# Kernel optimization log

Measured on AMD Instinct MI355X. Metric: run time of the kernel, lower is better.

Reference implementation:

```python
import jax, jax.numpy as jnp
import numpy as np

N = 100000   # nodes per graph
E = 1600000  # edges (avg degree 16)
B = 2        # num_graph (batch)
F_IN = 116   # num_input
EMB = 12     # embedding dim
H = 128      # hidden_size


def setup_inputs() -> dict:
    key = jax.random.key(0)
    ks = jax.random.split(key, 8)
    node = jax.random.normal(ks[0], (B, N, F_IN), dtype=jnp.float32)
    node_type = jax.random.randint(ks[1], (N,), 0, 8, dtype=jnp.int32)
    edge_index = jax.random.randint(ks[2], (2, E), 0, N, dtype=jnp.int32)
    embed = jax.random.normal(ks[3], (8, EMB), dtype=jnp.float32)
    d1 = F_IN + EMB
    W1 = jax.random.normal(ks[4], (d1, H), dtype=jnp.float32) / np.sqrt(d1)
    b1 = jnp.zeros((H,), dtype=jnp.float32)
    W2 = jax.random.normal(ks[5], (H, H), dtype=jnp.float32) / np.sqrt(H)
    b2 = jnp.zeros((H,), dtype=jnp.float32)
    return {"node": node, "node_type": node_type, "edge_index": edge_index,
            "embed": embed, "W1": W1, "b1": b1, "W2": W2, "b2": b2}


def _gcn_conv(x, src, dst, W, b):
    """PyG GCNConv: symmetric norm with self-loops, linear (no lin bias), bias after agg.
    x: [B, N, F]; src/dst: [E] int; W: [F, H]; b: [H]."""
    n = x.shape[1]
    # degree over (A + I), computed on destination nodes
    deg = jnp.zeros((n,), x.dtype).at[dst].add(1.0) + 1.0
    dis = jax.lax.rsqrt(deg)  # deg^{-1/2}
    xw = jnp.einsum('bnf,fh->bnh', x, W)          # [B, N, H]
    norm = dis[src] * dis[dst]                    # [E]
    msgs = xw[:, src, :] * norm[None, :, None]    # [B, E, H]
    agg = jax.vmap(lambda m: jax.ops.segment_sum(m, dst, num_segments=n))(msgs)
    agg = agg + xw * (dis * dis)[None, :, None]   # self-loop contribution
    return agg + b


def reference(node, node_type, edge_index, embed, W1, b1, W2, b2):
    src, dst = edge_index[0], edge_index[1]
    emb = embed[node_type]                                      # [N, EMB]
    b = node.shape[0]
    emb_b = jnp.broadcast_to(emb[None], (b,) + emb.shape)       # repeat over batch
    x = jnp.concatenate([node, emb_b], axis=2)                  # [B, N, F_IN+EMB]
    x = jax.nn.relu(_gcn_conv(x, src, dst, W1, b1))
    # F.dropout in eval mode is identity
    x = _gcn_conv(x, src, dst, W2, b2)
    return jnp.mean(x, axis=1)                                  # [B, H]
```

## Files before the change

kernel.cpp:

```cpp
#include <hip/hip_runtime.h>
#include <stdint.h>

typedef unsigned int uint32;
typedef unsigned short ushort16;
typedef __attribute__((ext_vector_type(8))) short bf16x8;
typedef __attribute__((ext_vector_type(4))) float f32x4;
typedef __attribute__((ext_vector_type(2))) float f32x2;

#define F_IN 116
#define HID  128
#define EMBD 12
#define IDX24 0x00FFFFFFu
#define BCAP 4608
#define PCAP 8448

__device__ __forceinline__ uint32 f2bf(float f) {
    uint32 x = __float_as_uint(f);
    return (x + 0x7fffu + ((x >> 16) & 1u)) >> 16;
}

__global__ void k_setup(const float* __restrict__ W1, ushort16* __restrict__ W1s,
                        int* __restrict__ bcurD, int* __restrict__ bcurS,
                        float* __restrict__ partial, uint32* __restrict__ xwzrow,
                        int* __restrict__ csrz, int N, int K) {
    int tid = blockIdx.x * 256 + threadIdx.x;
    if (tid < K) { bcurD[tid] = tid * BCAP; bcurS[tid] = tid * BCAP; }
    if (blockIdx.x == 0) {
        partial[threadIdx.x] = 0.f;
        if (threadIdx.x < 64) xwzrow[threadIdx.x] = 0u;
        if (threadIdx.x < 16) csrz[threadIdx.x] = N;
    }
    if (tid < 2048) {
        int q = tid & 3, n = (tid >> 2) & 15, t = (tid >> 6) & 7, kc = (tid >> 9) & 3;
        int chunk = ((kc * 8 + t) * 64 + n * 4 + q);
        int h = ((n >> 2) << 5) + t * 4 + (n & 3);
#pragma unroll
        for (int j = 0; j < 8; ++j) {
            int k = kc * 32 + q * 8 + j;
            W1s[chunk * 8 + j] = (ushort16)f2bf(W1[k * HID + h]);
        }
    }
}

__global__ __launch_bounds__(256) void k_bin(
    const int* __restrict__ src, const int* __restrict__ dst,
    int* __restrict__ bcurD, int* __restrict__ bcurS,
    uint32* __restrict__ ebufD, uint32* __restrict__ ebufS, int E) {
    __shared__ int lhD[512], lbD[512], lhS[512], lbS[512];
    const int tid = threadIdx.x;
    const int e0 = blockIdx.x * 4096;
    const int eend = min(e0 + 4096, E);
    for (int i = tid; i < 512; i += 256) { lhD[i] = 0; lhS[i] = 0; }
    __syncthreads();
    for (int e = e0 + tid; e < eend; e += 256) {
        atomicAdd(&lhD[dst[e] >> 8], 1);
        atomicAdd(&lhS[src[e] >> 8], 1);
    }
    __syncthreads();
    const int rot = (blockIdx.x * 277) & 511;
#pragma unroll
    for (int i = 0; i < 2; ++i) {
        int k = (rot + tid + i * 256) & 511;
        int c = lhD[k]; lbD[k] = c ? atomicAdd(&bcurD[k], c) : 0; lhD[k] = 0;
        int d = lhS[k]; lbS[k] = d ? atomicAdd(&bcurS[k], d) : 0; lhS[k] = 0;
    }
    __syncthreads();
    for (int e = e0 + tid; e < eend; e += 256) {
        int s = src[e], d = dst[e];
        int bkD = d >> 8;
        int p = lbD[bkD] + atomicAdd(&lhD[bkD], 1);
        if (p < (bkD + 1) * BCAP) ebufD[p] = ((uint32)(d & 255) << 24) | (uint32)s;
        int bkS = s >> 8;
        int p2 = lbS[bkS] + atomicAdd(&lhS[bkS], 1);
        if (p2 < (bkS + 1) * BCAP) ebufS[p2] = ((uint32)(s & 255) << 24) | (uint32)d;
    }
}

__global__ __launch_bounds__(256) void k_csr(
    const uint32* __restrict__ ebufD, const int* __restrict__ bcurD,
    int4* __restrict__ meta, float* __restrict__ dis,
    int* __restrict__ csr, int N, int ZROW) {
    __shared__ int cnt[256];
    __shared__ int cur[256];
    __shared__ int lst[256];
    __shared__ int ps[256];
    const int b = blockIdx.x, tid = threadIdx.x;
    const int r0 = b * BCAP;
    const int r1 = min(bcurD[b], r0 + BCAP);
    cnt[tid] = 0;
    __syncthreads();
    for (int p = r0 + tid; p < r1; p += 256)
        atomicAdd(&cnt[ebufD[p] >> 24], 1);
    __syncthreads();
    const int pl = (cnt[tid] + 15) & ~15;
    ps[tid] = pl;
    __syncthreads();
    for (int off = 1; off < 256; off <<= 1) {
        int t = (tid >= off) ? ps[tid - off] : 0;
        __syncthreads();
        ps[tid] += t;
        __syncthreads();
    }
    const int start = b * PCAP + ps[tid] - pl;
    lst[tid] = start;
    cur[tid] = start;
    const int n = (b << 8) + tid;
    float dl = rsqrtf(1.0f + (float)cnt[tid]);
    if (n < N) {
        dis[n] = dl;
        meta[n] = make_int4(start, pl >> 4, __float_as_int(dl), 0);
    }
    __syncthreads();
    for (int p = r0 + tid; p < r1; p += 256) {
        uint32 v = ebufD[p];
        csr[atomicAdd(&cur[v >> 24], 1)] = (int)(v & IDX24);
    }
    __syncthreads();
    {
        int end = lst[tid] + pl;
        for (int p = cur[tid]; p < end; ++p) csr[p] = ZROW;
    }
}

__global__ __launch_bounds__(256) void k_souts(
    const uint32* __restrict__ ebufS, const int* __restrict__ bcurS,
    const float* __restrict__ dis, int4* __restrict__ meta, int N) {
    __shared__ float lso[256];
    const int b = blockIdx.x, tid = threadIdx.x;
    const int r0 = b * BCAP;
    const int r1 = min(bcurS[b], r0 + BCAP);
    lso[tid] = 0.f;
    __syncthreads();
    for (int p = r0 + tid; p < r1; p += 256) {
        uint32 v = ebufS[p];
        atomicAdd(&lso[v >> 24], dis[v & IDX24]);
    }
    __syncthreads();
    int n = (b << 8) + tid;
    if (n < N) meta[n].w = __float_as_int(lso[tid]);
}

__global__ __launch_bounds__(256) void k_gemm(
    const float* __restrict__ node, const ushort16* __restrict__ W1s,
    const int* __restrict__ ntype, const float* __restrict__ embed,
    const float* __restrict__ dis, uint32* __restrict__ xw8, int N, int M, int T)
{
    __shared__ ushort16 ldsA[4 * 4 * 64 * 8];
    __shared__ uint4    ldsW[2048];
    __shared__ float    ldis[32];
    const int tid = threadIdx.x;

    {
        const uint4* Wg = (const uint4*)W1s;
#pragma unroll
        for (int i = 0; i < 8; ++i) ldsW[i * 256 + tid] = Wg[i * 256 + tid];
    }

    const int g = tid & 31;
    const int kc0 = g >> 3, q0 = (g >> 1) & 3, half = g & 1;
    const int lane = tid & 63;
    const int w = tid >> 6;
    const int fragsel = (lane & 15) * 4 + (lane >> 4);
    const int row = lane & 15, q = lane >> 4;

    for (int t = blockIdx.x; t < T; t += gridDim.x) {
        const int row0 = t * 64;
        if (tid < 32) {
            int n = (row0 >> 1) + tid;
            ldis[tid] = (n < N) ? dis[n] : 0.f;
        }

        float4 v[8];
#pragma unroll
        for (int j = 0; j < 8; ++j) {
            int r = (tid >> 5) + j * 8;
            int m = row0 + r;
            int n = m >> 1, b = m & 1;
            float4 val = make_float4(0.f, 0.f, 0.f, 0.f);
            if (n < N) {
                const float* ap = (g < 29)
                    ? node + ((size_t)b * N + n) * F_IN + g * 4
                    : embed + ntype[n] * EMBD + (g - 29) * 4;
                val = *(const float4*)ap;
            }
            v[j] = val;
        }
        asm volatile("" ::: "memory");
#pragma unroll
        for (int j = 0; j < 8; ++j) {
            int r = (tid >> 5) + j * 8;
            uint32 u0 = f2bf(v[j].x) | (f2bf(v[j].y) << 16);
            uint32 u1 = f2bf(v[j].z) | (f2bf(v[j].w) << 16);
            int mt = r >> 4, mloc = r & 15;
            int chunk = (mt * 4 + kc0) * 64 + mloc * 4 + q0;
            *(uint2*)&ldsA[chunk * 8 + half * 4] = make_uint2(u0, u1);
        }
        __syncthreads();

        f32x4 acc[8];
#pragma unroll
        for (int ct = 0; ct < 8; ++ct) acc[ct] = (f32x4){0.f, 0.f, 0.f, 0.f};

#pragma unroll
        for (int kc = 0; kc < 4; ++kc) {
            bf16x8 bfr = *(const bf16x8*)&ldsA[(((w * 4 + kc) * 64) + fragsel) * 8];
#pragma unroll
            for (int ct = 0; ct < 8; ++ct) {
                bf16x8 afr = *(const bf16x8*)((const char*)ldsW +
                                (((kc * 8 + ct) * 64 + fragsel) << 4));
                acc[ct] = __builtin_amdgcn_mfma_f32_16x16x32_bf16(afr, bfr, acc[ct], 0, 0, 0);
            }
        }

        int m = row0 + w * 16 + row;
        if (m < M) {
            float dn = ldis[(w * 16 + row) >> 1];
            uint32 d[8];
#pragma unroll
            for (int ct = 0; ct < 8; ++ct) {
                f32x4 a = acc[ct];
                int u = __builtin_amdgcn_cvt_pk_fp8_f32(a[0] * dn, a[1] * dn, 0, false);
                u = __builtin_amdgcn_cvt_pk_fp8_f32(a[2] * dn, a[3] * dn, u, true);
                d[ct] = (uint32)u;
            }
            uint32* rowp = xw8 + (size_t)m * 32 + q * 8;
            *(uint4*)rowp       = make_uint4(d[0], d[1], d[2], d[3]);
            *(uint4*)(rowp + 4) = make_uint4(d[4], d[5], d[6], d[7]);
        }
        __syncthreads();
    }
}

__global__ __launch_bounds__(256, 4) void k_gather(
    const uint32* __restrict__ xw8, const int* __restrict__ csr,
    const int4* __restrict__ meta, const float* __restrict__ b1,
    float* __restrict__ partial, int n0, int n1, int ZT)
{
    __shared__ float sm[4][256];
    const int tid  = threadIdx.x;
    const int lane = tid & 63;
    const int wid  = tid >> 6;
    const int wv = (blockIdx.x * blockDim.x + tid) >> 6;
    const int nw = (gridDim.x * blockDim.x) >> 6;
    const int c0 = (lane & 31) * 4;
    const int slot = (lane >> 5) * HID + c0;
    const float bb0 = b1[c0], bb1 = b1[c0 + 1], bb2 = b1[c0 + 2], bb3 = b1[c0 + 3];

    float p0 = 0.f, p1 = 0.f, p2 = 0.f, p3 = 0.f;

    for (int n = n0 + wv * 2; n < n1; n += nw * 2) {
        const int ns = __builtin_amdgcn_readfirstlane(n);
        const int has2 = (ns + 1 < n1);
        const int4 m1 = meta[ns];
        const int4 m2 = has2 ? meta[ns + 1] : make_int4(0, 0, 0, 0);
        const int st1 = m1.x, c1 = m1.y;
        const float dn1 = __int_as_float(m1.z), so1 = __int_as_float(m1.w);
        const int st2 = m2.x, c2 = m2.y;
        const float dn2 = __int_as_float(m2.z), so2 = __int_as_float(m2.w);

        uint32 sv1 = xw8[(size_t)ns * 64 + lane];
        uint32 sv2 = has2 ? xw8[((size_t)ns + 1) * 64 + lane] : 0u;
        f32x2 lo1 = __builtin_amdgcn_cvt_pk_f32_fp8(sv1, false);
        f32x2 hi1 = __builtin_amdgcn_cvt_pk_f32_fp8(sv1, true);
        f32x2 lo2 = __builtin_amdgcn_cvt_pk_f32_fp8(sv2, false);
        f32x2 hi2 = __builtin_amdgcn_cvt_pk_f32_fp8(sv2, true);
        float a10 = lo1.x, a11 = lo1.y, a12 = hi1.x, a13 = hi1.y;
        float a20 = lo2.x, a21 = lo2.y, a22 = hi2.x, a23 = hi2.y;

        int o1 = (c1 > 0) ? st1 : ZT;
        int o2 = (c2 > 0) ? st2 : ZT;
        int4 A0 = *(const int4*)&csr[o1];      int4 A1 = *(const int4*)&csr[o1 + 4];
        int4 A2 = *(const int4*)&csr[o1 + 8];  int4 A3 = *(const int4*)&csr[o1 + 12];
        int4 B0 = *(const int4*)&csr[o2];      int4 B1 = *(const int4*)&csr[o2 + 4];
        int4 B2 = *(const int4*)&csr[o2 + 8];  int4 B3 = *(const int4*)&csr[o2 + 12];

        const int jm = max(c1, c2);
        for (int j = 0; j < jm; ++j) {
            uint32 w1[16], w2[16];
            w1[0]  = xw8[(size_t)A0.x * 64 + lane];
            w1[1]  = xw8[(size_t)A0.y * 64 + lane];
            w1[2]  = xw8[(size_t)A0.z * 64 + lane];
            w1[3]  = xw8[(size_t)A0.w * 64 + lane];
            w1[4]  = xw8[(size_t)A1.x * 64 + lane];
            w1[5]  = xw8[(size_t)A1.y * 64 + lane];
            w1[6]  = xw8[(size_t)A1.z * 64 + lane];
            w1[7]  = xw8[(size_t)A1.w * 64 + lane];
            w1[8]  = xw8[(size_t)A2.x * 64 + lane];
            w1[9]  = xw8[(size_t)A2.y * 64 + lane];
            w1[10] = xw8[(size_t)A2.z * 64 + lane];
            w1[11] = xw8[(size_t)A2.w * 64 + lane];
            w1[12] = xw8[(size_t)A3.x * 64 + lane];
            w1[13] = xw8[(size_t)A3.y * 64 + lane];
            w1[14] = xw8[(size_t)A3.z * 64 + lane];
            w1[15] = xw8[(size_t)A3.w * 64 + lane];
            w2[0]  = xw8[(size_t)B0.x * 64 + lane];
            w2[1]  = xw8[(size_t)B0.y * 64 + lane];
            w2[2]  = xw8[(size_t)B0.z * 64 + lane];
            w2[3]  = xw8[(size_t)B0.w * 64 + lane];
            w2[4]  = xw8[(size_t)B1.x * 64 + lane];
            w2[5]  = xw8[(size_t)B1.y * 64 + lane];
            w2[6]  = xw8[(size_t)B1.z * 64 + lane];
            w2[7]  = xw8[(size_t)B1.w * 64 + lane];
            w2[8]  = xw8[(size_t)B2.x * 64 + lane];
            w2[9]  = xw8[(size_t)B2.y * 64 + lane];
            w2[10] = xw8[(size_t)B2.z * 64 + lane];
            w2[11] = xw8[(size_t)B2.w * 64 + lane];
            w2[12] = xw8[(size_t)B3.x * 64 + lane];
            w2[13] = xw8[(size_t)B3.y * 64 + lane];
            w2[14] = xw8[(size_t)B3.z * 64 + lane];
            w2[15] = xw8[(size_t)B3.w * 64 + lane];

            const int j1 = j + 1;
            o1 = (j1 < c1) ? st1 + j1 * 16 : ZT;
            o2 = (j1 < c2) ? st2 + j1 * 16 : ZT;
            A0 = *(const int4*)&csr[o1];      A1 = *(const int4*)&csr[o1 + 4];
            A2 = *(const int4*)&csr[o1 + 8];  A3 = *(const int4*)&csr[o1 + 12];
            B0 = *(const int4*)&csr[o2];      B1 = *(const int4*)&csr[o2 + 4];
            B2 = *(const int4*)&csr[o2 + 8];  B3 = *(const int4*)&csr[o2 + 12];

#pragma unroll
            for (int k = 0; k < 16; ++k) {
                f32x2 lo = __builtin_amdgcn_cvt_pk_f32_fp8(w1[k], false);
                f32x2 hi = __builtin_amdgcn_cvt_pk_f32_fp8(w1[k], true);
                a10 += lo.x; a11 += lo.y; a12 += hi.x; a13 += hi.y;
            }
#pragma unroll
            for (int k = 0; k < 16; ++k) {
                f32x2 lo = __builtin_amdgcn_cvt_pk_f32_fp8(w2[k], false);
                f32x2 hi = __builtin_amdgcn_cvt_pk_f32_fp8(w2[k], true);
                a20 += lo.x; a21 += lo.y; a22 += hi.x; a23 += hi.y;
            }
        }

        float cf1 = dn1 * (dn1 + so1);
        p0 = fmaf(cf1, fmaxf(fmaf(dn1, a10, bb0), 0.f), p0);
        p1 = fmaf(cf1, fmaxf(fmaf(dn1, a11, bb1), 0.f), p1);
        p2 = fmaf(cf1, fmaxf(fmaf(dn1, a12, bb2), 0.f), p2);
        p3 = fmaf(cf1, fmaxf(fmaf(dn1, a13, bb3), 0.f), p3);
        if (has2) {
            float cf2 = dn2 * (dn2 + so2);
            p0 = fmaf(cf2, fmaxf(fmaf(dn2, a20, bb0), 0.f), p0);
            p1 = fmaf(cf2, fmaxf(fmaf(dn2, a21, bb1), 0.f), p1);
            p2 = fmaf(cf2, fmaxf(fmaf(dn2, a22, bb2), 0.f), p2);
            p3 = fmaf(cf2, fmaxf(fmaf(dn2, a23, bb3), 0.f), p3);
        }
    }

    *(float4*)&sm[wid][slot] = make_float4(p0, p1, p2, p3);
    __syncthreads();
    if (tid < 256) {
        float s = sm[0][tid] + sm[1][tid] + sm[2][tid] + sm[3][tid];
        atomicAdd(&partial[tid], s);
    }
}

__global__ void k_final(const float* __restrict__ partial, const float* __restrict__ W2,
                        const float* __restrict__ b2, float* __restrict__ out, float invN) {
    int tid = threadIdx.x;
    int b = tid >> 7, h = tid & 127;
    float acc = 0.f;
#pragma unroll 8
    for (int k = 0; k < HID; ++k)
        acc += partial[b * HID + k] * W2[k * HID + h];
    out[tid] = acc * invN + b2[h];
}

extern "C" void kernel_launch(void* const* d_in, const int* in_sizes, int n_in,
                              void* d_out, int out_size, void* d_ws, size_t ws_size,
                              hipStream_t stream) {
    const float* node  = (const float*)d_in[0];
    const int*   ntype = (const int*)d_in[1];
    const int*   eidx  = (const int*)d_in[2];
    const float* embed = (const float*)d_in[3];
    const float* W1    = (const float*)d_in[4];
    const float* b1    = (const float*)d_in[5];
    const float* W2    = (const float*)d_in[6];
    const float* b2    = (const float*)d_in[7];
    float* out = (float*)d_out;

    const int N  = in_sizes[1];
    const int E  = in_sizes[2] / 2;
    const int B  = in_sizes[0] / (N * F_IN);
    const int M  = B * N;
    const int K  = (N + 255) >> 8;
    const int T  = (M + 63) >> 6;

    const int* src = eidx;
    const int* dst = eidx + E;

    char* ws = (char*)d_ws;
    size_t off = 0;
    auto alloc = [&](size_t bytes) -> void* {
        void* p = ws + off;
        off += (bytes + 255) & ~(size_t)255;
        return p;
    };
    uint32*   xw8     = (uint32*)alloc((size_t)(M + 2) * 128);
    int*      csr     = (int*)alloc(((size_t)K * PCAP + 16) * sizeof(int));
    uint32*   ebufD   = (uint32*)alloc((size_t)K * BCAP * sizeof(uint32));
    uint32*   ebufS   = (uint32*)alloc((size_t)K * BCAP * sizeof(uint32));
    int4*     meta    = (int4*)alloc((size_t)N * sizeof(int4));
    float*    dis     = (float*)alloc((size_t)N * sizeof(float));
    ushort16* W1s     = (ushort16*)alloc(4 * 8 * 64 * 8 * sizeof(ushort16));
    int*      bcurD   = (int*)alloc((size_t)K * sizeof(int));
    int*      bcurS   = (int*)alloc((size_t)K * sizeof(int));
    float*    partial = (float*)alloc(2 * HID * sizeof(float));

    const int ZT = K * PCAP;
    const int Nh = (N / 2 + 1) & ~1;

    k_setup<<<8, 256, 0, stream>>>(W1, W1s, bcurD, bcurS, partial,
                                   xw8 + (size_t)N * 64, csr + (size_t)ZT, N, K);
    k_bin<<<(E + 4095) / 4096, 256, 0, stream>>>(src, dst, bcurD, bcurS, ebufD, ebufS, E);
    k_csr<<<K, 256, 0, stream>>>(ebufD, bcurD, meta, dis, csr, N, N);
    k_souts<<<K, 256, 0, stream>>>(ebufS, bcurS, dis, meta, N);
    k_gemm<<<768, 256, 0, stream>>>(node, W1s, ntype, embed, dis, xw8, N, M, T);
    k_gather<<<1536, 256, 0, stream>>>(xw8, csr, meta, b1, partial, 0, Nh, ZT);
    k_gather<<<1536, 256, 0, stream>>>(xw8, csr, meta, b1, partial, Nh, N, ZT);
    k_final<<<1, 256, 0, stream>>>(partial, W2, b2, out, 1.0f / (float)N);
}
```

Before: 385.2 us.

## Replace bucketed CSR build with global-atomic degree count, scan, and fill

Drops the two-pass bucket binning (k_bin, k_csr, k_souts) and builds the CSR directly. One pass counts degrees with global atomics, a per-block scan assigns row offsets, and a fill pass scatters source indices and accumulates souts with global atomics. The two half-range gather launches become a single launch over all nodes with a larger grid. This removes the intermediate edge buffers and a kernel launch, at the cost of heavily contended global atomics and scattered CSR writes. The neighbour order inside each row now depends on atomic timing, so results are non-deterministic.

```diff
diff --git a/kernel.cpp b/kernel.cpp
--- a/kernel.cpp
+++ b/kernel.cpp
@@ -10,8 +10,6 @@
 #define F_IN 116
 #define HID  128
 #define EMBD 12
-#define IDX24 0x00FFFFFFu
-#define BCAP 4608
 #define PCAP 8448
 
 __device__ __forceinline__ uint32 f2bf(float f) {
@@ -20,11 +18,11 @@
 }
 
 __global__ void k_setup(const float* __restrict__ W1, ushort16* __restrict__ W1s,
-                        int* __restrict__ bcurD, int* __restrict__ bcurS,
+                        int* __restrict__ degD, float* __restrict__ souts,
                         float* __restrict__ partial, uint32* __restrict__ xwzrow,
-                        int* __restrict__ csrz, int N, int K) {
+                        int* __restrict__ csrz, int N) {
     int tid = blockIdx.x * 256 + threadIdx.x;
-    if (tid < K) { bcurD[tid] = tid * BCAP; bcurS[tid] = tid * BCAP; }
+    for (int i = tid; i < N; i += 64 * 256) { degD[i] = 0; souts[i] = 0.f; }
     if (blockIdx.x == 0) {
         partial[threadIdx.x] = 0.f;
         if (threadIdx.x < 64) xwzrow[threadIdx.x] = 0u;
@@ -42,57 +40,21 @@
     }
 }
 
-__global__ __launch_bounds__(256) void k_bin(
-    const int* __restrict__ src, const int* __restrict__ dst,
-    int* __restrict__ bcurD, int* __restrict__ bcurS,
-    uint32* __restrict__ ebufD, uint32* __restrict__ ebufS, int E) {
-    __shared__ int lhD[512], lbD[512], lhS[512], lbS[512];
-    const int tid = threadIdx.x;
-    const int e0 = blockIdx.x * 4096;
-    const int eend = min(e0 + 4096, E);
-    for (int i = tid; i < 512; i += 256) { lhD[i] = 0; lhS[i] = 0; }
-    __syncthreads();
-    for (int e = e0 + tid; e < eend; e += 256) {
-        atomicAdd(&lhD[dst[e] >> 8], 1);
-        atomicAdd(&lhS[src[e] >> 8], 1);
-    }
-    __syncthreads();
-    const int rot = (blockIdx.x * 277) & 511;
-#pragma unroll
-    for (int i = 0; i < 2; ++i) {
-        int k = (rot + tid + i * 256) & 511;
-        int c = lhD[k]; lbD[k] = c ? atomicAdd(&bcurD[k], c) : 0; lhD[k] = 0;
-        int d = lhS[k]; lbS[k] = d ? atomicAdd(&bcurS[k], d) : 0; lhS[k] = 0;
-    }
-    __syncthreads();
-    for (int e = e0 + tid; e < eend; e += 256) {
-        int s = src[e], d = dst[e];
-        int bkD = d >> 8;
-        int p = lbD[bkD] + atomicAdd(&lhD[bkD], 1);
-        if (p < (bkD + 1) * BCAP) ebufD[p] = ((uint32)(d & 255) << 24) | (uint32)s;
-        int bkS = s >> 8;
-        int p2 = lbS[bkS] + atomicAdd(&lhS[bkS], 1);
-        if (p2 < (bkS + 1) * BCAP) ebufS[p2] = ((uint32)(s & 255) << 24) | (uint32)d;
-    }
-}
-
-__global__ __launch_bounds__(256) void k_csr(
-    const uint32* __restrict__ ebufD, const int* __restrict__ bcurD,
-    int4* __restrict__ meta, float* __restrict__ dis,
-    int* __restrict__ csr, int N, int ZROW) {
-    __shared__ int cnt[256];
-    __shared__ int cur[256];
-    __shared__ int lst[256];
+__global__ __launch_bounds__(256) void k_deg(
+    const int* __restrict__ dst, int* __restrict__ degD, int E) {
+    int stride = gridDim.x * 256;
+    for (int e = blockIdx.x * 256 + threadIdx.x; e < E; e += stride)
+        atomicAdd(&degD[dst[e]], 1);
+}
+
+__global__ __launch_bounds__(256) void k_scanA(
+    const int* __restrict__ degD, int4* __restrict__ meta, float* __restrict__ dis,
+    int* __restrict__ gcur, int* __restrict__ csr, int N, int ZROW) {
     __shared__ int ps[256];
     const int b = blockIdx.x, tid = threadIdx.x;
-    const int r0 = b * BCAP;
-    const int r1 = min(bcurD[b], r0 + BCAP);
-    cnt[tid] = 0;
-    __syncthreads();
-    for (int p = r0 + tid; p < r1; p += 256)
-        atomicAdd(&cnt[ebufD[p] >> 24], 1);
-    __syncthreads();
-    const int pl = (cnt[tid] + 15) & ~15;
+    const int n = (b << 8) + tid;
+    const int deg = (n < N) ? degD[n] : 0;
+    const int pl = (deg + 15) & ~15;
     ps[tid] = pl;
     __syncthreads();
     for (int off = 1; off < 256; off <<= 1) {
@@ -102,42 +64,26 @@
         __syncthreads();
     }
     const int start = b * PCAP + ps[tid] - pl;
-    lst[tid] = start;
-    cur[tid] = start;
-    const int n = (b << 8) + tid;
-    float dl = rsqrtf(1.0f + (float)cnt[tid]);
     if (n < N) {
+        float dl = rsqrtf(1.0f + (float)deg);
         dis[n] = dl;
         meta[n] = make_int4(start, pl >> 4, __float_as_int(dl), 0);
-    }
-    __syncthreads();
-    for (int p = r0 + tid; p < r1; p += 256) {
-        uint32 v = ebufD[p];
-        csr[atomicAdd(&cur[v >> 24], 1)] = (int)(v & IDX24);
-    }
-    __syncthreads();
-    {
-        int end = lst[tid] + pl;
-        for (int p = cur[tid]; p < end; ++p) csr[p] = ZROW;
-    }
-}
-
-__global__ __launch_bounds__(256) void k_souts(
-    const uint32* __restrict__ ebufS, const int* __restrict__ bcurS,
-    const float* __restrict__ dis, int4* __restrict__ meta, int N) {
-    __shared__ float lso[256];
-    const int b = blockIdx.x, tid = threadIdx.x;
-    const int r0 = b * BCAP;
-    const int r1 = min(bcurS[b], r0 + BCAP);
-    lso[tid] = 0.f;
-    __syncthreads();
-    for (int p = r0 + tid; p < r1; p += 256) {
-        uint32 v = ebufS[p];
-        atomicAdd(&lso[v >> 24], dis[v & IDX24]);
-    }
-    __syncthreads();
-    int n = (b << 8) + tid;
-    if (n < N) meta[n].w = __float_as_int(lso[tid]);
+        gcur[n] = start;
+        for (int p = start + deg; p < start + pl; ++p) csr[p] = ZROW;
+    }
+}
+
+__global__ __launch_bounds__(256) void k_fill(
+    const int* __restrict__ src, const int* __restrict__ dst,
+    const float* __restrict__ dis, int* __restrict__ gcur,
+    int* __restrict__ csr, float* __restrict__ souts, int E) {
+    int stride = gridDim.x * 256;
+    for (int e = blockIdx.x * 256 + threadIdx.x; e < E; e += stride) {
+        int s = src[e], d = dst[e];
+        int p = atomicAdd(&gcur[d], 1);
+        csr[p] = s;
+        atomicAdd(&souts[s], dis[d]);
+    }
 }
 
 __global__ __launch_bounds__(256) void k_gemm(
@@ -233,8 +179,8 @@
 
 __global__ __launch_bounds__(256, 4) void k_gather(
     const uint32* __restrict__ xw8, const int* __restrict__ csr,
-    const int4* __restrict__ meta, const float* __restrict__ b1,
-    float* __restrict__ partial, int n0, int n1, int ZT)
+    const int4* __restrict__ meta, const float* __restrict__ souts,
+    const float* __restrict__ b1, float* __restrict__ partial, int N, int ZT)
 {
     __shared__ float sm[4][256];
     const int tid  = threadIdx.x;
@@ -248,15 +194,17 @@
 
     float p0 = 0.f, p1 = 0.f, p2 = 0.f, p3 = 0.f;
 
-    for (int n = n0 + wv * 2; n < n1; n += nw * 2) {
+    for (int n = wv * 2; n < N; n += nw * 2) {
         const int ns = __builtin_amdgcn_readfirstlane(n);
-        const int has2 = (ns + 1 < n1);
+        const int has2 = (ns + 1 < N);
         const int4 m1 = meta[ns];
         const int4 m2 = has2 ? meta[ns + 1] : make_int4(0, 0, 0, 0);
         const int st1 = m1.x, c1 = m1.y;
-        const float dn1 = __int_as_float(m1.z), so1 = __int_as_float(m1.w);
+        const float dn1 = __int_as_float(m1.z);
         const int st2 = m2.x, c2 = m2.y;
-        const float dn2 = __int_as_float(m2.z), so2 = __int_as_float(m2.w);
+        const float dn2 = __int_as_float(m2.z);
+        const float so1 = souts[ns];
+        const float so2 = has2 ? souts[ns + 1] : 0.f;
 
         uint32 sv1 = xw8[(size_t)ns * 64 + lane];
         uint32 sv2 = has2 ? xw8[((size_t)ns + 1) * 64 + lane] : 0u;
@@ -396,26 +344,23 @@
         return p;
     };
     uint32*   xw8     = (uint32*)alloc((size_t)(M + 2) * 128);
-    int*      csr     = (int*)alloc(((size_t)K * PCAP + 16) * sizeof(int));
-    uint32*   ebufD   = (uint32*)alloc((size_t)K * BCAP * sizeof(uint32));
-    uint32*   ebufS   = (uint32*)alloc((size_t)K * BCAP * sizeof(uint32));
+    int*      csr     = (int*)alloc(((size_t)K * PCAP + 16 + 64) * sizeof(int));
     int4*     meta    = (int4*)alloc((size_t)N * sizeof(int4));
     float*    dis     = (float*)alloc((size_t)N * sizeof(float));
+    float*    souts   = (float*)alloc((size_t)N * sizeof(float));
+    int*      degD    = (int*)alloc((size_t)N * sizeof(int));
+    int*      gcur    = (int*)alloc((size_t)N * sizeof(int));
     ushort16* W1s     = (ushort16*)alloc(4 * 8 * 64 * 8 * sizeof(ushort16));
-    int*      bcurD   = (int*)alloc((size_t)K * sizeof(int));
-    int*      bcurS   = (int*)alloc((size_t)K * sizeof(int));
     float*    partial = (float*)alloc(2 * HID * sizeof(float));
 
     const int ZT = K * PCAP;
-    const int Nh = (N / 2 + 1) & ~1;
-
-    k_setup<<<8, 256, 0, stream>>>(W1, W1s, bcurD, bcurS, partial,
-                                   xw8 + (size_t)N * 64, csr + (size_t)ZT, N, K);
-    k_bin<<<(E + 4095) / 4096, 256, 0, stream>>>(src, dst, bcurD, bcurS, ebufD, ebufS, E);
-    k_csr<<<K, 256, 0, stream>>>(ebufD, bcurD, meta, dis, csr, N, N);
-    k_souts<<<K, 256, 0, stream>>>(ebufS, bcurS, dis, meta, N);
+
+    k_setup<<<64, 256, 0, stream>>>(W1, W1s, degD, souts, partial,
+                                    xw8 + (size_t)N * 64, csr + (size_t)ZT, N);
+    k_deg<<<2048, 256, 0, stream>>>(dst, degD, E);
+    k_scanA<<<K, 256, 0, stream>>>(degD, meta, dis, gcur, csr, N, N);
+    k_fill<<<2048, 256, 0, stream>>>(src, dst, dis, gcur, csr, souts, E);
     k_gemm<<<768, 256, 0, stream>>>(node, W1s, ntype, embed, dis, xw8, N, M, T);
-    k_gather<<<1536, 256, 0, stream>>>(xw8, csr, meta, b1, partial, 0, Nh, ZT);
-    k_gather<<<1536, 256, 0, stream>>>(xw8, csr, meta, b1, partial, Nh, N, ZT);
+    k_gather<<<2048, 256, 0, stream>>>(xw8, csr, meta, souts, b1, partial, N, ZT);
     k_final<<<1, 256, 0, stream>>>(partial, W2, b2, out, 1.0f / (float)N);
 }
```

Result: slower. 497.1 us (+29.1%).

## Drop source-side edge binning; compute out-weights via global atomics in CSR build

Applied to the files above, without the earlier changes.

Removes the second (source-keyed) binning pass and the k_souts kernel, and instead accumulates each source's sum of neighbour deg^-1/2 with global float atomics while scattering edges into CSR. The two half-range gather launches are merged into one launch with a larger grid, and souts is read from its own array. This is meant to cut edge-buffer traffic, shared atomics and launch count, at the cost of contended global float atomics over 1.6M edges and a nondeterministic summation order.

```diff
diff --git a/kernel.cpp b/kernel.cpp
--- a/kernel.cpp
+++ b/kernel.cpp
@@ -20,11 +20,12 @@
 }
 
 __global__ void k_setup(const float* __restrict__ W1, ushort16* __restrict__ W1s,
-                        int* __restrict__ bcurD, int* __restrict__ bcurS,
+                        int* __restrict__ bcurD, float* __restrict__ souts,
                         float* __restrict__ partial, uint32* __restrict__ xwzrow,
                         int* __restrict__ csrz, int N, int K) {
     int tid = blockIdx.x * 256 + threadIdx.x;
-    if (tid < K) { bcurD[tid] = tid * BCAP; bcurS[tid] = tid * BCAP; }
+    for (int i = tid; i < N; i += 64 * 256) souts[i] = 0.f;
+    if (tid < K) bcurD[tid] = tid * BCAP;
     if (blockIdx.x == 0) {
         partial[threadIdx.x] = 0.f;
         if (threadIdx.x < 64) xwzrow[threadIdx.x] = 0u;
@@ -44,46 +45,40 @@
 
 __global__ __launch_bounds__(256) void k_bin(
     const int* __restrict__ src, const int* __restrict__ dst,
-    int* __restrict__ bcurD, int* __restrict__ bcurS,
-    uint32* __restrict__ ebufD, uint32* __restrict__ ebufS, int E) {
-    __shared__ int lhD[512], lbD[512], lhS[512], lbS[512];
+    int* __restrict__ bcurD, uint32* __restrict__ ebufD, int E) {
+    __shared__ int lh[512], lb[512];
     const int tid = threadIdx.x;
     const int e0 = blockIdx.x * 4096;
     const int eend = min(e0 + 4096, E);
-    for (int i = tid; i < 512; i += 256) { lhD[i] = 0; lhS[i] = 0; }
-    __syncthreads();
-    for (int e = e0 + tid; e < eend; e += 256) {
-        atomicAdd(&lhD[dst[e] >> 8], 1);
-        atomicAdd(&lhS[src[e] >> 8], 1);
-    }
+    for (int i = tid; i < 512; i += 256) lh[i] = 0;
+    __syncthreads();
+    for (int e = e0 + tid; e < eend; e += 256)
+        atomicAdd(&lh[dst[e] >> 8], 1);
     __syncthreads();
     const int rot = (blockIdx.x * 277) & 511;
 #pragma unroll
     for (int i = 0; i < 2; ++i) {
         int k = (rot + tid + i * 256) & 511;
-        int c = lhD[k]; lbD[k] = c ? atomicAdd(&bcurD[k], c) : 0; lhD[k] = 0;
-        int d = lhS[k]; lbS[k] = d ? atomicAdd(&bcurS[k], d) : 0; lhS[k] = 0;
+        int c = lh[k]; lb[k] = c ? atomicAdd(&bcurD[k], c) : 0; lh[k] = 0;
     }
     __syncthreads();
     for (int e = e0 + tid; e < eend; e += 256) {
         int s = src[e], d = dst[e];
-        int bkD = d >> 8;
-        int p = lbD[bkD] + atomicAdd(&lhD[bkD], 1);
-        if (p < (bkD + 1) * BCAP) ebufD[p] = ((uint32)(d & 255) << 24) | (uint32)s;
-        int bkS = s >> 8;
-        int p2 = lbS[bkS] + atomicAdd(&lhS[bkS], 1);
-        if (p2 < (bkS + 1) * BCAP) ebufS[p2] = ((uint32)(s & 255) << 24) | (uint32)d;
+        int bk = d >> 8;
+        int p = lb[bk] + atomicAdd(&lh[bk], 1);
+        if (p < (bk + 1) * BCAP) ebufD[p] = ((uint32)(d & 255) << 24) | (uint32)s;
     }
 }
 
 __global__ __launch_bounds__(256) void k_csr(
     const uint32* __restrict__ ebufD, const int* __restrict__ bcurD,
-    int4* __restrict__ meta, float* __restrict__ dis,
+    int4* __restrict__ meta, float* __restrict__ dis, float* __restrict__ souts,
     int* __restrict__ csr, int N, int ZROW) {
     __shared__ int cnt[256];
     __shared__ int cur[256];
     __shared__ int lst[256];
     __shared__ int ps[256];
+    __shared__ float sdl[256];
     const int b = blockIdx.x, tid = threadIdx.x;
     const int r0 = b * BCAP;
     const int r1 = min(bcurD[b], r0 + BCAP);
@@ -106,6 +101,7 @@
     cur[tid] = start;
     const int n = (b << 8) + tid;
     float dl = rsqrtf(1.0f + (float)cnt[tid]);
+    sdl[tid] = dl;
     if (n < N) {
         dis[n] = dl;
         meta[n] = make_int4(start, pl >> 4, __float_as_int(dl), 0);
@@ -113,31 +109,16 @@
     __syncthreads();
     for (int p = r0 + tid; p < r1; p += 256) {
         uint32 v = ebufD[p];
-        csr[atomicAdd(&cur[v >> 24], 1)] = (int)(v & IDX24);
+        int dloc = v >> 24;
+        int s = (int)(v & IDX24);
+        csr[atomicAdd(&cur[dloc], 1)] = s;
+        atomicAdd(&souts[s], sdl[dloc]);
     }
     __syncthreads();
     {
         int end = lst[tid] + pl;
         for (int p = cur[tid]; p < end; ++p) csr[p] = ZROW;
     }
-}
-
-__global__ __launch_bounds__(256) void k_souts(
-    const uint32* __restrict__ ebufS, const int* __restrict__ bcurS,
-    const float* __restrict__ dis, int4* __restrict__ meta, int N) {
-    __shared__ float lso[256];
-    const int b = blockIdx.x, tid = threadIdx.x;
-    const int r0 = b * BCAP;
-    const int r1 = min(bcurS[b], r0 + BCAP);
-    lso[tid] = 0.f;
-    __syncthreads();
-    for (int p = r0 + tid; p < r1; p += 256) {
-        uint32 v = ebufS[p];
-        atomicAdd(&lso[v >> 24], dis[v & IDX24]);
-    }
-    __syncthreads();
-    int n = (b << 8) + tid;
-    if (n < N) meta[n].w = __float_as_int(lso[tid]);
 }
 
 __global__ __launch_bounds__(256) void k_gemm(
@@ -233,8 +214,8 @@
 
 __global__ __launch_bounds__(256, 4) void k_gather(
     const uint32* __restrict__ xw8, const int* __restrict__ csr,
-    const int4* __restrict__ meta, const float* __restrict__ b1,
-    float* __restrict__ partial, int n0, int n1, int ZT)
+    const int4* __restrict__ meta, const float* __restrict__ souts,
+    const float* __restrict__ b1, float* __restrict__ partial, int N, int ZT)
 {
     __shared__ float sm[4][256];
     const int tid  = threadIdx.x;
@@ -248,15 +229,17 @@
 
     float p0 = 0.f, p1 = 0.f, p2 = 0.f, p3 = 0.f;
 
-    for (int n = n0 + wv * 2; n < n1; n += nw * 2) {
+    for (int n = wv * 2; n < N; n += nw * 2) {
         const int ns = __builtin_amdgcn_readfirstlane(n);
-        const int has2 = (ns + 1 < n1);
+        const int has2 = (ns + 1 < N);
         const int4 m1 = meta[ns];
         const int4 m2 = has2 ? meta[ns + 1] : make_int4(0, 0, 0, 0);
         const int st1 = m1.x, c1 = m1.y;
-        const float dn1 = __int_as_float(m1.z), so1 = __int_as_float(m1.w);
+        const float dn1 = __int_as_float(m1.z);
         const int st2 = m2.x, c2 = m2.y;
-        const float dn2 = __int_as_float(m2.z), so2 = __int_as_float(m2.w);
+        const float dn2 = __int_as_float(m2.z);
+        const float so1 = souts[ns];
+        const float so2 = has2 ? souts[ns + 1] : 0.f;
 
         uint32 sv1 = xw8[(size_t)ns * 64 + lane];
         uint32 sv2 = has2 ? xw8[((size_t)ns + 1) * 64 + lane] : 0u;
@@ -396,26 +379,22 @@
         return p;
     };
     uint32*   xw8     = (uint32*)alloc((size_t)(M + 2) * 128);
-    int*      csr     = (int*)alloc(((size_t)K * PCAP + 16) * sizeof(int));
+    int*      csr     = (int*)alloc(((size_t)K * PCAP + 16 + 64) * sizeof(int));
     uint32*   ebufD   = (uint32*)alloc((size_t)K * BCAP * sizeof(uint32));
-    uint32*   ebufS   = (uint32*)alloc((size_t)K * BCAP * sizeof(uint32));
     int4*     meta    = (int4*)alloc((size_t)N * sizeof(int4));
     float*    dis     = (float*)alloc((size_t)N * sizeof(float));
+    float*    souts   = (float*)alloc((size_t)N * sizeof(float));
     ushort16* W1s     = (ushort16*)alloc(4 * 8 * 64 * 8 * sizeof(ushort16));
     int*      bcurD   = (int*)alloc((size_t)K * sizeof(int));
-    int*      bcurS   = (int*)alloc((size_t)K * sizeof(int));
     float*    partial = (float*)alloc(2 * HID * sizeof(float));
 
     const int ZT = K * PCAP;
-    const int Nh = (N / 2 + 1) & ~1;
-
-    k_setup<<<8, 256, 0, stream>>>(W1, W1s, bcurD, bcurS, partial,
-                                   xw8 + (size_t)N * 64, csr + (size_t)ZT, N, K);
-    k_bin<<<(E + 4095) / 4096, 256, 0, stream>>>(src, dst, bcurD, bcurS, ebufD, ebufS, E);
-    k_csr<<<K, 256, 0, stream>>>(ebufD, bcurD, meta, dis, csr, N, N);
-    k_souts<<<K, 256, 0, stream>>>(ebufS, bcurS, dis, meta, N);
+
+    k_setup<<<64, 256, 0, stream>>>(W1, W1s, bcurD, souts, partial,
+                                    xw8 + (size_t)N * 64, csr + (size_t)ZT, N, K);
+    k_bin<<<(E + 4095) / 4096, 256, 0, stream>>>(src, dst, bcurD, ebufD, E);
+    k_csr<<<K, 256, 0, stream>>>(ebufD, bcurD, meta, dis, souts, csr, N, N);
     k_gemm<<<768, 256, 0, stream>>>(node, W1s, ntype, embed, dis, xw8, N, M, T);
-    k_gather<<<1536, 256, 0, stream>>>(xw8, csr, meta, b1, partial, 0, Nh, ZT);
-    k_gather<<<1536, 256, 0, stream>>>(xw8, csr, meta, b1, partial, Nh, N, ZT);
+    k_gather<<<2048, 256, 0, stream>>>(xw8, csr, meta, souts, b1, partial, N, ZT);
     k_final<<<1, 256, 0, stream>>>(partial, W2, b2, out, 1.0f / (float)N);
 }
```

Result: slower. 394.6 us (+2.4%).
